# Kernel optimization log

Hardware: AMD Instinct MI355X
Metric: run time of the kernel (lower is better)

Reference implementation:

```python
import jax, jax.numpy as jnp
import numpy as np

B, N = 4, 2048
VD, CD = 256, 64
H = 4
INNER = VD  # inner_ratio = 1
D = INNER // H  # head_dim = 64
EPS = 1e-5
RMS_EPS = 1e-6


def layer_norm(x, g, b):
    m = jnp.mean(x, axis=-1, keepdims=True)
    v = jnp.mean((x - m) ** 2, axis=-1, keepdims=True)
    return (x - m) * jax.lax.rsqrt(v + EPS) * g + b


def rms_norm(x, s):
    ms = jnp.mean(x * x, axis=-1, keepdims=True)
    return x * jax.lax.rsqrt(ms + RMS_EPS) * s


def split_heads(x):  # (b, n, h*d) -> (b, h, n, d)
    b, n, _ = x.shape
    return x.reshape(b, n, H, D).transpose(0, 2, 1, 3)


def setup_inputs() -> dict:
    key = jax.random.key(0)
    ks = jax.random.split(key, 10)
    w = lambda k, shp: jax.random.normal(k, shp, dtype=jnp.float32) * 0.02
    return {
        "V": jax.random.normal(ks[0], (B, N, VD), dtype=jnp.float32),
        "C": jax.random.normal(ks[1], (B, N, CD), dtype=jnp.float32),
        "vn_g": jnp.ones((VD,), jnp.float32), "vn_b": jnp.zeros((VD,), jnp.float32),
        "cn_g": jnp.ones((CD,), jnp.float32), "cn_b": jnp.zeros((CD,), jnp.float32),
        "W_vqk": w(ks[2], (VD, 2 * INNER)), "b_vqk": jnp.zeros((2 * INNER,), jnp.float32),
        "rms_v": jnp.ones((2 * INNER,), jnp.float32),
        "W_cqk": w(ks[3], (CD, 2 * INNER)), "b_cqk": jnp.zeros((2 * INNER,), jnp.float32),
        "rms_c": jnp.ones((2 * INNER,), jnp.float32),
        "W_vv": w(ks[4], (VD, INNER)), "b_vv": jnp.zeros((INNER,), jnp.float32),
        "W_cv": w(ks[5], (CD, INNER)), "b_cv": jnp.zeros((INNER,), jnp.float32),
        "W_ov": w(ks[6], (INNER, VD)), "b_ov": jnp.zeros((VD,), jnp.float32),
        "W_oc": w(ks[7], (INNER, CD)), "b_oc": jnp.zeros((CD,), jnp.float32),
    }


def reference(V, C, vn_g, vn_b, cn_g, cn_b, W_vqk, b_vqk, rms_v, W_cqk, b_cqk, rms_c,
              W_vv, b_vv, W_cv, b_cv, W_ov, b_ov, W_oc, b_oc):
    Vn = layer_norm(V, vn_g, vn_b)
    Cn = layer_norm(C, cn_g, cn_b)
    qkv = rms_norm(Vn @ W_vqk + b_vqk, rms_v)
    qkc = rms_norm(Cn @ W_cqk + b_cqk, rms_c)
    qv, kv = jnp.split(qkv, 2, axis=-1)
    qc, kc = jnp.split(qkc, 2, axis=-1)
    vv = Vn @ W_vv + b_vv
    vc = Cn @ W_cv + b_cv
    qv, kv, vv, qc, kc, vc = map(split_heads, (qv, kv, vv, qc, kc, vc))
    # shared attention map: softmax((QvKv^T + QcKc^T)/sqrt(d))
    scores = (jnp.einsum("bhnd,bhmd->bhnm", qv, kv)
              + jnp.einsum("bhnd,bhmd->bhnm", qc, kc)) / np.sqrt(D).astype(np.float32)
    attn = jax.nn.softmax(scores, axis=-1)
    out_v = jnp.einsum("bhnm,bhmd->bhnd", attn, vv).transpose(0, 2, 1, 3).reshape(B, N, INNER)
    out_c = jnp.einsum("bhnm,bhmd->bhnd", attn, vc).transpose(0, 2, 1, 3).reshape(B, N, INNER)
    return out_v @ W_ov + b_ov, out_c @ W_oc + b_oc
```

## Files before the change

kernel.cpp:

```cpp
#include <hip/hip_runtime.h>

typedef unsigned short u16;
typedef unsigned int   u32;
typedef short s16x8 __attribute__((ext_vector_type(8)));
typedef float f32x4 __attribute__((ext_vector_type(4)));

#define WS_STATSV 0
#define WS_STATSC 65536
#define WS_WT_VQK 131072
#define WS_WT_CQK 393216
#define WS_WT_VV  458752
#define WS_WT_CV  589824
#define WS_WT_OV  622592
#define WS_WT_OC  753664
#define WS_Q      786432
#define WS_K      9175040
#define WS_VT     17563648
#define WS_OV     25952256
#define WS_OC     30146560

__device__ __forceinline__ float bf2f(u16 h){
  union { u32 u; float f; } x; x.u = ((u32)h) << 16; return x.f;
}
__device__ __forceinline__ u16 f2bf(float f){
  union { float f; u32 u; } x; x.f = f;
  u32 u = x.u; u += 0x7fffu + ((u >> 16) & 1u);
  return (u16)(u >> 16);
}
__device__ __forceinline__ f32x4 mfma16(s16x8 a, s16x8 b, f32x4 c){
  return __builtin_amdgcn_mfma_f32_16x16x32_bf16(a, b, c, 0, 0, 0);
}
__device__ __forceinline__ void async16(const u16* g, u16* l){
  __builtin_amdgcn_global_load_lds(
      (const __attribute__((address_space(1))) u32*)(const void*)g,
      (__attribute__((address_space(3))) u32*)(void*)l, 16, 0, 0);
}

__global__ __launch_bounds__(256) void k_prep(const float* V, const float* C,
    const float* Wvqk, const float* Wcqk, const float* Wvv, const float* Wcv,
    const float* Wov, const float* Woc, char* ws){
  int bid = blockIdx.x;
  if (bid < 4096){
    int wid = threadIdx.x >> 6, lane = threadIdx.x & 63;
    float2* sV = (float2*)(ws + WS_STATSV);
    float2* sC = (float2*)(ws + WS_STATSC);
    float s = 0.f, s2 = 0.f; int row; float2* dst; float invn;
    if (bid < 2048){
      row = bid*4 + wid;
      const float4* p = (const float4*)(V + row*256);
      float4 v = p[lane];
      s = v.x+v.y+v.z+v.w; s2 = v.x*v.x+v.y*v.y+v.z*v.z+v.w*v.w;
      dst = sV; invn = 1.0f/256.0f;
    } else {
      row = (bid-2048)*4 + wid;
      float x = C[row*64 + lane];
      s = x; s2 = x*x;
      dst = sC; invn = 1.0f/64.0f;
    }
    for (int d=1; d<64; d<<=1){ s += __shfl_xor(s,d); s2 += __shfl_xor(s2,d); }
    if (lane == 0){
      float m = s*invn; float var = s2*invn - m*m; if (var < 0.f) var = 0.f;
      float rstd = rsqrtf(var + 1e-5f);
      float2 o; o.x = rstd; o.y = -m*rstd;
      dst[row] = o;
    }
  } else {
    int tb = bid - 4096;
    const float* src; u16* dst; int K, N, rel;
    if      (tb <  64){ src=Wvqk; dst=(u16*)(ws+WS_WT_VQK); K=256; N=512; rel=tb;     }
    else if (tb <  80){ src=Wcqk; dst=(u16*)(ws+WS_WT_CQK); K=64;  N=512; rel=tb-64;  }
    else if (tb < 112){ src=Wvv;  dst=(u16*)(ws+WS_WT_VV);  K=256; N=256; rel=tb-80;  }
    else if (tb < 120){ src=Wcv;  dst=(u16*)(ws+WS_WT_CV);  K=64;  N=256; rel=tb-112; }
    else if (tb < 152){ src=Wov;  dst=(u16*)(ws+WS_WT_OV);  K=256; N=256; rel=tb-120; }
    else              { src=Woc;  dst=(u16*)(ws+WS_WT_OC);  K=256; N=64;  rel=tb-152; }
    int e = rel*2048 + threadIdx.x*8;
    int k = e / N, n0 = e % N;
    float4 t0 = *(const float4*)(src + e);
    float4 t1 = *(const float4*)(src + e + 4);
    dst[(n0+0)*K + k] = f2bf(t0.x);
    dst[(n0+1)*K + k] = f2bf(t0.y);
    dst[(n0+2)*K + k] = f2bf(t0.z);
    dst[(n0+3)*K + k] = f2bf(t0.w);
    dst[(n0+4)*K + k] = f2bf(t1.x);
    dst[(n0+5)*K + k] = f2bf(t1.y);
    dst[(n0+6)*K + k] = f2bf(t1.z);
    dst[(n0+7)*K + k] = f2bf(t1.w);
  }
}

__device__ __forceinline__ s16x8 ln_frag(const float* A, const float* g, const float* bb,
                                         int base, int k0, float2 stt){
  float4 x0 = *(const float4*)(A + base + k0);
  float4 x1 = *(const float4*)(A + base + k0 + 4);
  float4 g0 = *(const float4*)(g + k0);
  float4 g1 = *(const float4*)(g + k0 + 4);
  float4 b0 = *(const float4*)(bb + k0);
  float4 b1 = *(const float4*)(bb + k0 + 4);
  s16x8 af;
  af[0] = (short)f2bf(fmaf(fmaf(x0.x, stt.x, stt.y), g0.x, b0.x));
  af[1] = (short)f2bf(fmaf(fmaf(x0.y, stt.x, stt.y), g0.y, b0.y));
  af[2] = (short)f2bf(fmaf(fmaf(x0.z, stt.x, stt.y), g0.z, b0.z));
  af[3] = (short)f2bf(fmaf(fmaf(x0.w, stt.x, stt.y), g0.w, b0.w));
  af[4] = (short)f2bf(fmaf(fmaf(x1.x, stt.x, stt.y), g1.x, b1.x));
  af[5] = (short)f2bf(fmaf(fmaf(x1.y, stt.x, stt.y), g1.y, b1.y));
  af[6] = (short)f2bf(fmaf(fmaf(x1.z, stt.x, stt.y), g1.z, b1.z));
  af[7] = (short)f2bf(fmaf(fmaf(x1.w, stt.x, stt.y), g1.w, b1.w));
  return af;
}

__global__ __launch_bounds__(256) void k_proj(const float* V, const float* C,
    const float* vg, const float* vb, const float* cgam, const float* cbet,
    const float* bvqk, const float* bcqk, const float* rmsv, const float* rmsc,
    const float* bvv, const float* bcv, char* ws){
  __shared__ float ssl[4][16];
  int bid = blockIdx.x;
  int tid = threadIdx.x, lane = tid & 63, w = tid >> 6;
  int c = lane & 15, q = lane >> 4;

  if (bid < 1024){
    bool csd = bid >= 512;
    int rb = (bid & 511) * 16;
    const float* A   = csd ? C : V;
    int K            = csd ? 64 : 256;
    const float2* st = (const float2*)(ws + (csd ? WS_STATSC : WS_STATSV));
    const float* g   = csd ? cgam : vg;
    const float* bb  = csd ? cbet : vb;
    const u16* Wt    = (const u16*)(ws + (csd ? WS_WT_CQK : WS_WT_VQK));
    const float* bias= csd ? bcqk : bvqk;
    const float* rms = csd ? rmsc : rmsv;
    int dOff         = csd ? 64 : 0;

    int row = rb + c;
    float2 stt = st[row];
    int j0 = w * 128;

    f32x4 acc[8];
    #pragma unroll
    for (int f=0; f<8; f++){ f32x4 z = {0.f,0.f,0.f,0.f}; acc[f] = z; }

    int nkc = K >> 5;
    for (int kc=0; kc<nkc; kc++){
      int k0 = kc*32 + q*8;
      s16x8 af = ln_frag(A, g, bb, row*K, k0, stt);
      #pragma unroll
      for (int f=0; f<8; f++){
        s16x8 bfr = *(const s16x8*)(Wt + (j0 + f*16 + c)*K + k0);
        acc[f] = mfma16(af, bfr, acc[f]);
      }
    }

    float ss[4] = {0.f,0.f,0.f,0.f};
    float rsv[8];
    #pragma unroll
    for (int f=0; f<8; f++){
      int j = j0 + f*16 + c;
      float bsv = bias[j]; rsv[f] = rms[j];
      #pragma unroll
      for (int i=0;i<4;i++){ acc[f][i] += bsv; ss[i] += acc[f][i]*acc[f][i]; }
    }
    #pragma unroll
    for (int d=1; d<16; d<<=1){
      #pragma unroll
      for (int i=0;i<4;i++) ss[i] += __shfl_xor(ss[i], d);
    }
    if (c == 0){
      #pragma unroll
      for (int i=0;i<4;i++) ssl[w][q*4 + i] = ss[i];
    }
    __syncthreads();
    float rmsr[4];
    #pragma unroll
    for (int i=0;i<4;i++){
      int rl = q*4 + i;
      float tot = ssl[0][rl] + ssl[1][rl] + ssl[2][rl] + ssl[3][rl];
      rmsr[i] = rsqrtf(tot * (1.0f/512.0f) + 1e-6f);
    }
    u16* dstb = (u16*)(ws + (w < 2 ? WS_Q : WS_K));
    float qs = (w < 2) ? 0.125f*1.44269504f : 1.0f;
    #pragma unroll
    for (int f=0; f<8; f++){
      int jj = (j0 + f*16 + c) & 255;
      int head = jj >> 6, dd = (jj & 63) + dOff;
      #pragma unroll
      for (int i=0;i<4;i++){
        int r = rb + q*4 + i;
        int b_ = r >> 11, n = r & 2047;
        dstb[((b_*4 + head)*2048 + n)*128 + dd] = f2bf(acc[f][i]*rmsr[i]*rsv[f]*qs);
      }
    }
  } else {
    int vb2 = bid - 1024;
    bool csd = vb2 >= 256;
    int rb = (vb2 & 255) * 32;
    const float* A   = csd ? C : V;
    int K            = csd ? 64 : 256;
    const float2* st = (const float2*)(ws + (csd ? WS_STATSC : WS_STATSV));
    const float* g   = csd ? cgam : vg;
    const float* bb  = csd ? cbet : vb;
    const u16* Wt    = (const u16*)(ws + (csd ? WS_WT_CV : WS_WT_VV));
    const float* bias= csd ? bcv : bvv;
    int dOff         = csd ? 64 : 0;

    int s = w & 1, cgp = w >> 1;
    int r0 = rb + s*16, row = r0 + c;
    float2 stt = st[row];
    int j0 = cgp * 128;

    f32x4 acc[8];
    #pragma unroll
    for (int f=0; f<8; f++){ f32x4 z = {0.f,0.f,0.f,0.f}; acc[f] = z; }

    int nkc = K >> 5;
    for (int kc=0; kc<nkc; kc++){
      int k0 = kc*32 + q*8;
      s16x8 af = ln_frag(A, g, bb, row*K, k0, stt);
      #pragma unroll
      for (int f=0; f<8; f++){
        s16x8 bfr = *(const s16x8*)(Wt + (j0 + f*16 + c)*K + k0);
        acc[f] = mfma16(af, bfr, acc[f]);
      }
    }
    u16* vt = (u16*)(ws + WS_VT);
    int r = r0 + q*4;
    int b_ = r >> 11, n = r & 2047;
    #pragma unroll
    for (int f=0; f<8; f++){
      int j = j0 + f*16 + c;
      float bv_ = bias[j];
      int head = j >> 6, dd = (j & 63) + dOff;
      ushort4 pk;
      pk.x = f2bf(acc[f][0] + bv_); pk.y = f2bf(acc[f][1] + bv_);
      pk.z = f2bf(acc[f][2] + bv_); pk.w = f2bf(acc[f][3] + bv_);
      *(ushort4*)(vt + ((b_*4 + head)*128 + dd)*2048 + n) = pk;
    }
  }
}

__global__ __launch_bounds__(256, 2) void k_attn(char* ws){
  const u16* Qw = (const u16*)(ws + WS_Q);
  const u16* Kw = (const u16*)(ws + WS_K);
  const u16* Vt = (const u16*)(ws + WS_VT);
  u16* Ov = (u16*)(ws + WS_OV);
  u16* Oc = (u16*)(ws + WS_OC);
  __shared__ char smem[75776];
  u16* sm16 = (u16*)smem;

  int bh = blockIdx.x & 15, qb = blockIdx.x >> 4;
  int tid = threadIdx.x, lane = tid & 63, w = tid >> 6;
  int c = lane & 15, q = lane >> 4;
  int g = w & 1, h = w >> 1, ht = tid & 127;
  int qr0 = qb*64 + g*32;

  s16x8 qf[2][4];
  #pragma unroll
  for (int s=0;s<2;s++)
    #pragma unroll
    for (int kc=0;kc<4;kc++)
      qf[s][kc] = *(const s16x8*)(Qw + (bh*2048 + qr0 + s*16 + c)*128 + kc*32 + q*8);

  const u16* ksrc[4]; const u16* vsrc[4];
  #pragma unroll
  for (int i=0;i<4;i++){
    int sc = i*128 + ht;
    { int r = sc >> 4, j = (sc & 15) ^ (r & 15);
      ksrc[i] = Kw + (bh*2048 + r)*128 + j*8; }
    { int r = sc >> 2, j = (sc & 3) ^ ((r >> 1) & 3);
      vsrc[i] = Vt + (bh*128 + r)*2048 + j*8; }
  }

  f32x4 o[2][8];
  float lsum[2][4];
  #pragma unroll
  for (int s=0;s<2;s++){
    #pragma unroll
    for (int f8=0;f8<8;f8++){ f32x4 z = {0.f,0.f,0.f,0.f}; o[s][f8] = z; }
    #pragma unroll
    for (int i=0;i<4;i++) lsum[s][i] = 0.f;
  }

  auto stage = [&](int buf, int t){
    u16* kd = sm16 + (h*2+buf)*4096;
    u16* vd = sm16 + 16384 + (h*2+buf)*4096;
    #pragma unroll
    for (int i=0;i<4;i++){
      async16(ksrc[i] + t*4096, kd + (i*128+ht)*8);
      async16(vsrc[i] + t*32,   vd + (i*128+ht)*8);
    }
  };

  auto step = [&](int bi, int tt){
    int t = h*32 + tt;
    __syncthreads();
    if (tt < 31) stage(bi^1, t+1);

    const u16* kb = sm16 + (h*2+bi)*4096;
    const u16* vb = sm16 + 16384 + (h*2+bi)*4096;
    s16x8 kf[2][4];
    #pragma unroll
    for (int f=0;f<2;f++)
      #pragma unroll
      for (int kc=0;kc<4;kc++)
        kf[f][kc] = *(const s16x8*)(kb + ((f*16+c)*16 + (((kc*4+q) ^ c) & 15))*8);
    s16x8 vf[8];
    #pragma unroll
    for (int f8=0;f8<8;f8++)
      vf[f8] = *(const s16x8*)(vb + ((f8*16+c)*4 + ((q ^ ((c>>1)&3)) & 3))*8);

    f32x4 sfr[2][2];
    #pragma unroll
    for (int s=0;s<2;s++)
      #pragma unroll
      for (int f=0;f<2;f++){ f32x4 z = {0.f,0.f,0.f,0.f}; sfr[s][f] = z; }
    #pragma unroll
    for (int s=0;s<2;s++)
      #pragma unroll
      for (int f=0;f<2;f++)
        #pragma unroll
        for (int kc=0;kc<4;kc++)
          sfr[s][f] = mfma16(qf[s][kc], kf[f][kc], sfr[s][f]);

    #pragma unroll
    for (int s=0;s<2;s++){
      u16* ps = sm16 + 32768 + (w*2+s)*640;
      #pragma unroll
      for (int f=0;f<2;f++){
        #pragma unroll
        for (int i=0;i<4;i++){
          float p = exp2f(sfr[s][f][i]);
          lsum[s][i] += p;
          ps[(q*4 + i)*40 + f*16 + c] = f2bf(p);
        }
      }
      s16x8 pf = *(const s16x8*)(ps + c*40 + q*8);
      #pragma unroll
      for (int f8=0;f8<8;f8++)
        o[s][f8] = mfma16(pf, vf[f8], o[s][f8]);
    }
  };

  stage(0, h*32);
  for (int tt=0; tt<32; tt+=2){
    step(0, tt);
    step(1, tt+1);
  }

  __syncthreads();
  float* mg = (float*)smem;
  if (h == 1){
    float* d = mg + (g*64 + lane)*73;
    #pragma unroll
    for (int s=0;s<2;s++)
      #pragma unroll
      for (int f8=0;f8<8;f8++)
        #pragma unroll
        for (int i=0;i<4;i++) d[(s*8+f8)*4 + i] = o[s][f8][i];
    #pragma unroll
    for (int s=0;s<2;s++)
      #pragma unroll
      for (int i=0;i<4;i++) d[64 + s*4 + i] = lsum[s][i];
  }
  __syncthreads();
  if (h == 0){
    float* d = mg + (g*64 + lane)*73;
    #pragma unroll
    for (int s=0;s<2;s++)
      #pragma unroll
      for (int f8=0;f8<8;f8++)
        #pragma unroll
        for (int i=0;i<4;i++) o[s][f8][i] += d[(s*8+f8)*4 + i];
    #pragma unroll
    for (int s=0;s<2;s++)
      #pragma unroll
      for (int i=0;i<4;i++) lsum[s][i] += d[64 + s*4 + i];

    #pragma unroll
    for (int dd=1; dd<16; dd<<=1)
      #pragma unroll
      for (int s=0;s<2;s++)
        #pragma unroll
        for (int i=0;i<4;i++) lsum[s][i] += __shfl_xor(lsum[s][i], dd);

    int b_ = bh >> 2, hh = bh & 3;
    #pragma unroll
    for (int s=0;s<2;s++){
      float inv[4];
      #pragma unroll
      for (int i=0;i<4;i++) inv[i] = 1.0f/lsum[s][i];
      #pragma unroll
      for (int f8=0;f8<8;f8++){
        int col = f8*16 + c;
        u16* dst = (col < 64) ? Ov : Oc;
        int ddim = col & 63;
        #pragma unroll
        for (int i=0;i<4;i++){
          int n = qr0 + s*16 + q*4 + i;
          dst[(b_*2048 + n)*256 + hh*64 + ddim] = f2bf(o[s][f8][i]*inv[i]);
        }
      }
    }
  }
}

__global__ __launch_bounds__(256) void k_out(const u16* Av, const u16* Wtv, const float* bv,
                                             const u16* Ac, const u16* Wtc, const float* bc,
                                             float* out){
  int bid = blockIdx.x;
  int tid = threadIdx.x, lane = tid & 63, w = tid >> 6;
  int c = lane & 15, q = lane >> 4;
  if (bid < 512){
    int rb = bid * 16;
    int row = rb + c;
    int j0 = w * 64;
    f32x4 acc[4];
    #pragma unroll
    for (int f=0; f<4; f++){ f32x4 z = {0.f,0.f,0.f,0.f}; acc[f] = z; }
    for (int kc=0; kc<8; kc++){
      int k0 = kc*32 + q*8;
      s16x8 af = *(const s16x8*)(Av + row*256 + k0);
      #pragma unroll
      for (int f=0; f<4; f++){
        s16x8 bfr = *(const s16x8*)(Wtv + (j0 + f*16 + c)*256 + k0);
        acc[f] = mfma16(af, bfr, acc[f]);
      }
    }
    #pragma unroll
    for (int f=0; f<4; f++){
      int j = j0 + f*16 + c;
      float bb = bv[j];
      #pragma unroll
      for (int i=0;i<4;i++)
        out[(rb + q*4 + i)*256 + j] = acc[f][i] + bb;
    }
  } else {
    int rb = (bid - 512) * 64;
    int r0 = rb + w*16, row = r0 + c;
    f32x4 acc[4];
    #pragma unroll
    for (int f=0; f<4; f++){ f32x4 z = {0.f,0.f,0.f,0.f}; acc[f] = z; }
    for (int kc=0; kc<8; kc++){
      int k0 = kc*32 + q*8;
      s16x8 af = *(const s16x8*)(Ac + row*256 + k0);
      #pragma unroll
      for (int f=0; f<4; f++){
        s16x8 bfr = *(const s16x8*)(Wtc + (f*16 + c)*256 + k0);
        acc[f] = mfma16(af, bfr, acc[f]);
      }
    }
    float* oc = out + 2097152;
    #pragma unroll
    for (int f=0; f<4; f++){
      int j = f*16 + c;
      float bb = bc[j];
      #pragma unroll
      for (int i=0;i<4;i++)
        oc[(r0 + q*4 + i)*64 + j] = acc[f][i] + bb;
    }
  }
}

extern "C" void kernel_launch(void* const* d_in, const int* in_sizes, int n_in,
                              void* d_out, int out_size, void* d_ws, size_t ws_size,
                              hipStream_t stream){
  (void)in_sizes; (void)n_in; (void)out_size; (void)ws_size;
  const float* V    = (const float*)d_in[0];
  const float* C    = (const float*)d_in[1];
  const float* vng  = (const float*)d_in[2];
  const float* vnb  = (const float*)d_in[3];
  const float* cng  = (const float*)d_in[4];
  const float* cnb  = (const float*)d_in[5];
  const float* Wvqk = (const float*)d_in[6];
  const float* bvqk = (const float*)d_in[7];
  const float* rmsv = (const float*)d_in[8];
  const float* Wcqk = (const float*)d_in[9];
  const float* bcqk = (const float*)d_in[10];
  const float* rmsc = (const float*)d_in[11];
  const float* Wvv  = (const float*)d_in[12];
  const float* bvv  = (const float*)d_in[13];
  const float* Wcv  = (const float*)d_in[14];
  const float* bcv  = (const float*)d_in[15];
  const float* Wov  = (const float*)d_in[16];
  const float* bov  = (const float*)d_in[17];
  const float* Woc  = (const float*)d_in[18];
  const float* boc  = (const float*)d_in[19];
  char* ws = (char*)d_ws;
  float* out = (float*)d_out;

  k_prep<<<4256, 256, 0, stream>>>(V, C, Wvqk, Wcqk, Wvv, Wcv, Wov, Woc, ws);
  k_proj<<<1536, 256, 0, stream>>>(V, C, vng, vnb, cng, cnb,
                                   bvqk, bcqk, rmsv, rmsc, bvv, bcv, ws);
  k_attn<<<512, 256, 0, stream>>>(ws);
  k_out<<<640, 256, 0, stream>>>((const u16*)(ws + WS_OV), (const u16*)(ws + WS_WT_OV), bov,
                                 (const u16*)(ws + WS_OC), (const u16*)(ws + WS_WT_OC), boc,
                                 out);
}
```

Baseline: 219.3 us.

## Compute transposed scores to keep P in registers, permute V layout

The QK^T MFMA now runs with operands swapped, so each lane holds scores for one query row across keys. The probabilities can then be packed straight into the A-operand fragment for the PV MFMA, dropping the LDS write/read round trip for P. To match the new key ordering inside the packed fragment, the V-projection kernel writes V^T with a permuted sequence index within each 32-key block. The row-sum reduction becomes a per-lane scalar with cross-quad shuffles, and shared memory shrinks since the P scratch buffer is gone.

```diff
diff --git a/kernel.cpp b/kernel.cpp
--- a/kernel.cpp
+++ b/kernel.cpp
@@ -223,6 +223,8 @@
     u16* vt = (u16*)(ws + WS_VT);
     int r = r0 + q*4;
     int b_ = r >> 11, n = r & 2047;
+    int m = n & 31;
+    int nper = (n & ~31) | (((m & 15) >> 2)*8 + (m >> 4)*4);
     #pragma unroll
     for (int f=0; f<8; f++){
       int j = j0 + f*16 + c;
@@ -231,7 +233,7 @@
       ushort4 pk;
       pk.x = f2bf(acc[f][0] + bv_); pk.y = f2bf(acc[f][1] + bv_);
       pk.z = f2bf(acc[f][2] + bv_); pk.w = f2bf(acc[f][3] + bv_);
-      *(ushort4*)(vt + ((b_*4 + head)*128 + dd)*2048 + n) = pk;
+      *(ushort4*)(vt + ((b_*4 + head)*128 + dd)*2048 + nper) = pk;
     }
   }
 }
@@ -242,7 +244,7 @@
   const u16* Vt = (const u16*)(ws + WS_VT);
   u16* Ov = (u16*)(ws + WS_OV);
   u16* Oc = (u16*)(ws + WS_OC);
-  __shared__ char smem[75776];
+  __shared__ char smem[65536];
   u16* sm16 = (u16*)smem;
 
   int bh = blockIdx.x & 15, qb = blockIdx.x >> 4;
@@ -269,14 +271,11 @@
   }
 
   f32x4 o[2][8];
-  float lsum[2][4];
+  float lsum[2] = {0.f, 0.f};
   #pragma unroll
-  for (int s=0;s<2;s++){
+  for (int s=0;s<2;s++)
     #pragma unroll
     for (int f8=0;f8<8;f8++){ f32x4 z = {0.f,0.f,0.f,0.f}; o[s][f8] = z; }
-    #pragma unroll
-    for (int i=0;i<4;i++) lsum[s][i] = 0.f;
-  }
 
   auto stage = [&](int buf, int t){
     u16* kd = sm16 + (h*2+buf)*4096;
@@ -317,24 +316,23 @@
       for (int f=0;f<2;f++)
         #pragma unroll
         for (int kc=0;kc<4;kc++)
-          sfr[s][f] = mfma16(qf[s][kc], kf[f][kc], sfr[s][f]);
+          sfr[s][f] = mfma16(kf[f][kc], qf[s][kc], sfr[s][f]);
 
     #pragma unroll
     for (int s=0;s<2;s++){
-      u16* ps = sm16 + 32768 + (w*2+s)*640;
-      #pragma unroll
-      for (int f=0;f<2;f++){
-        #pragma unroll
-        for (int i=0;i<4;i++){
-          float p = exp2f(sfr[s][f][i]);
-          lsum[s][i] += p;
-          ps[(q*4 + i)*40 + f*16 + c] = f2bf(p);
-        }
-      }
-      s16x8 pf = *(const s16x8*)(ps + c*40 + q*8);
+      float p0 = exp2f(sfr[s][0][0]), p1 = exp2f(sfr[s][0][1]);
+      float p2 = exp2f(sfr[s][0][2]), p3 = exp2f(sfr[s][0][3]);
+      float p4 = exp2f(sfr[s][1][0]), p5 = exp2f(sfr[s][1][1]);
+      float p6 = exp2f(sfr[s][1][2]), p7 = exp2f(sfr[s][1][3]);
+      lsum[s] += ((p0+p1)+(p2+p3)) + ((p4+p5)+(p6+p7));
+      union { u32 u[4]; s16x8 v; } pa;
+      pa.u[0] = (u32)f2bf(p0) | ((u32)f2bf(p1) << 16);
+      pa.u[1] = (u32)f2bf(p2) | ((u32)f2bf(p3) << 16);
+      pa.u[2] = (u32)f2bf(p4) | ((u32)f2bf(p5) << 16);
+      pa.u[3] = (u32)f2bf(p6) | ((u32)f2bf(p7) << 16);
       #pragma unroll
       for (int f8=0;f8<8;f8++)
-        o[s][f8] = mfma16(pf, vf[f8], o[s][f8]);
+        o[s][f8] = mfma16(pa.v, vf[f8], o[s][f8]);
     }
   };
 
@@ -347,45 +345,38 @@
   __syncthreads();
   float* mg = (float*)smem;
   if (h == 1){
-    float* d = mg + (g*64 + lane)*73;
+    float* d = mg + (g*64 + lane)*67;
     #pragma unroll
     for (int s=0;s<2;s++)
       #pragma unroll
       for (int f8=0;f8<8;f8++)
         #pragma unroll
         for (int i=0;i<4;i++) d[(s*8+f8)*4 + i] = o[s][f8][i];
-    #pragma unroll
-    for (int s=0;s<2;s++)
-      #pragma unroll
-      for (int i=0;i<4;i++) d[64 + s*4 + i] = lsum[s][i];
+    d[64] = lsum[0]; d[65] = lsum[1];
   }
   __syncthreads();
   if (h == 0){
-    float* d = mg + (g*64 + lane)*73;
+    float* d = mg + (g*64 + lane)*67;
     #pragma unroll
     for (int s=0;s<2;s++)
       #pragma unroll
       for (int f8=0;f8<8;f8++)
         #pragma unroll
         for (int i=0;i<4;i++) o[s][f8][i] += d[(s*8+f8)*4 + i];
-    #pragma unroll
-    for (int s=0;s<2;s++)
-      #pragma unroll
-      for (int i=0;i<4;i++) lsum[s][i] += d[64 + s*4 + i];
-
-    #pragma unroll
-    for (int dd=1; dd<16; dd<<=1)
-      #pragma unroll
-      for (int s=0;s<2;s++)
-        #pragma unroll
-        for (int i=0;i<4;i++) lsum[s][i] += __shfl_xor(lsum[s][i], dd);
+    lsum[0] += d[64]; lsum[1] += d[65];
+
+    #pragma unroll
+    for (int s=0;s<2;s++){
+      lsum[s] += __shfl_xor(lsum[s], 16);
+      lsum[s] += __shfl_xor(lsum[s], 32);
+    }
 
     int b_ = bh >> 2, hh = bh & 3;
     #pragma unroll
     for (int s=0;s<2;s++){
       float inv[4];
       #pragma unroll
-      for (int i=0;i<4;i++) inv[i] = 1.0f/lsum[s][i];
+      for (int i=0;i<4;i++) inv[i] = 1.0f/__shfl(lsum[s], q*4 + i);
       #pragma unroll
       for (int f8=0;f8<8;f8++){
         int col = f8*16 + c;
```

After: 215.1 us. No clear change (-1.9%).
